# Optimization experiments

Measured on AMD Instinct MI355X. Metric: run time of the kernel, lower is better.

## Reference

```python
import jax, jax.numpy as jnp
import numpy as np

G = 32        # grid points per axis (in_p is a regular [0,1]^3 grid)
M = 8         # half n_modes (n_modes=16 -> keep 8 low + 8 high per dim, 8 in rfft dim)
NL = 4        # fno_n_layers
HID = 64      # fno_hidden_channels
LIFT = 256    # fno_lifting_channels
NOUT = 16384  # number of output query points
RADIUS = 0.033


def setup_inputs() -> dict:
    key = jax.random.key(0)
    ks = jax.random.split(key, 16)
    g = jnp.linspace(0.0, 1.0, G)
    X, Y, Z = jnp.meshgrid(g, g, g, indexing='ij')
    in_p = jnp.stack([X, Y, Z], -1).astype(jnp.float32)            # [G,G,G,3]
    f = jax.random.normal(ks[0], (G, G, G, 3), jnp.float32)        # [G,G,G,3]
    out_p = jax.random.uniform(ks[1], (NOUT, 3), dtype=jnp.float32)

    def lin(k, i, o):
        return jax.random.normal(k, (i, o), jnp.float32) * (float(i) ** -0.5)

    inp = {
        'in_p': in_p, 'out_p': out_p, 'f': f,
        # Lifting MLP: (in_channels+3)=6 -> 256 -> 64
        'lift_w1': lin(ks[2], 6, LIFT), 'lift_b1': jnp.zeros((LIFT,), jnp.float32),
        'lift_w2': lin(ks[3], LIFT, HID), 'lift_b2': jnp.zeros((HID,), jnp.float32),
        # Spectral weights: [layer, corner(4), in, out, M, M, M, (re,im)]
        'spec_w': jax.random.normal(ks[4], (NL, 4, HID, HID, M, M, M, 2), jnp.float32) * 0.02,
        # Linear (soft) skip per layer
        'skip_w': jax.random.normal(ks[5], (NL, HID, HID), jnp.float32) * (float(HID) ** -0.5),
        'skip_b': jnp.zeros((NL, HID), jnp.float32),
        # GNO kernel MLP: 6 -> 512 -> 256 -> 64
        'gno_w1': lin(ks[6], 6, 512), 'gno_b1': jnp.zeros((512,), jnp.float32),
        'gno_w2': lin(ks[7], 512, 256), 'gno_b2': jnp.zeros((256,), jnp.float32),
        'gno_w3': lin(ks[8], 256, HID), 'gno_b3': jnp.zeros((HID,), jnp.float32),
        # Projection: 64 -> 256 -> 1
        'proj_w1': lin(ks[9], HID, 256), 'proj_b1': jnp.zeros((256,), jnp.float32),
        'proj_w2': lin(ks[10], 256, 1), 'proj_b2': jnp.zeros((1,), jnp.float32),
    }
    return inp


def reference(in_p, out_p, f, lift_w1, lift_b1, lift_w2, lift_b2, spec_w,
              skip_w, skip_b, gno_w1, gno_b1, gno_w2, gno_b2, gno_w3, gno_b3,
              proj_w1, proj_b1, proj_w2, proj_b2):
    gelu = lambda x: jax.nn.gelu(x, approximate=False)

    # ---- FNO latent embedding (channels-last) ----
    h = jnp.concatenate([f, in_p], -1)                               # [G,G,G,6]
    h = gelu(h @ lift_w1 + lift_b1) @ lift_w2 + lift_b2              # [G,G,G,HID]

    w = spec_w[..., 0] + 1j * spec_w[..., 1]                         # [NL,4,i,o,M,M,M]
    lo, hi = slice(0, M), slice(-M, None)
    corners = [(lo, lo), (lo, hi), (hi, lo), (hi, hi)]
    sz = slice(0, M)
    for l in range(NL):
        ft = jnp.fft.rfftn(h, axes=(0, 1, 2), norm='forward')        # [G,G,G//2+1,HID]
        out_ft = jnp.zeros_like(ft)
        for c, (sx, sy) in enumerate(corners):
            blk = jnp.einsum('xyzi,ioxyz->xyzo', ft[sx, sy, sz], w[l, c])
            out_ft = out_ft.at[sx, sy, sz].set(blk)
        hs = jnp.fft.irfftn(out_ft, s=(G, G, G), axes=(0, 1, 2), norm='forward')
        h = hs + h @ skip_w[l] + skip_b[l]
        if l < NL - 1:
            h = gelu(h)
    latent = h.reshape(-1, HID)                                      # [G^3, HID]

    # ---- GNO: radius neighbor search on regular grid + gather-MLP-mean ----
    hgrid = 1.0 / (G - 1)
    i0 = jnp.round(out_p * (G - 1)).astype(jnp.int32)                # nearest cell [N,3]
    off = jnp.stack(jnp.meshgrid(*([jnp.arange(-1, 2)] * 3), indexing='ij'), -1).reshape(-1, 3)
    cand = i0[:, None, :] + off[None]                                # [N,27,3]
    inb = jnp.all((cand >= 0) & (cand < G), -1)
    cc = jnp.clip(cand, 0, G - 1)
    flat = (cc[..., 0] * G + cc[..., 1]) * G + cc[..., 2]            # [N,27]
    ycoord = cc.astype(jnp.float32) * hgrid                          # neighbor coords
    d2 = jnp.sum((out_p[:, None, :] - ycoord) ** 2, -1)
    mask = inb & (d2 <= RADIUS * RADIUS)

    # kernel input = cat([y_coords, x_coords]) per edge -> MLP -> k(x,y) [N,27,HID]
    agg = jnp.concatenate([ycoord, jnp.broadcast_to(out_p[:, None, :], ycoord.shape)], -1)
    k = gelu(agg @ gno_w1 + gno_b1)
    k = gelu(k @ gno_w2 + gno_b2)
    k = k @ gno_w3 + gno_b3
    fy = latent[flat]                                                # gather [N,27,HID]
    msk = mask[..., None].astype(k.dtype)
    num = jnp.sum(k * fy * msk, axis=1)
    den = jnp.maximum(jnp.sum(msk, axis=1), 1.0)
    out = num / den                                                  # [N,HID] (mean reduce)

    # ---- Projection ----
    out = gelu(out @ proj_w1 + proj_b1) @ proj_w2 + proj_b2          # [N,1]
    return out
```

## Files before the change

### kernel.cpp

```cpp
#include <hip/hip_runtime.h>
#include <math.h>


#define ECAP 131072

typedef _Float16 f16x8 __attribute__((ext_vector_type(8)));
typedef float f32x4 __attribute__((ext_vector_type(4)));

__device__ __forceinline__ float gelu_f(float x) {
    float t = fabsf(x) * 0.7071067811865475f;
    float k = __builtin_amdgcn_rcpf(1.0f + 0.3275911f * t);
    float e = __expf(-t * t);
    float y = k*(0.254829592f + k*(-0.284496736f + k*(1.421413741f +
              k*(-1.453152027f + k*1.061405429f))));
    float erfv = 1.0f - y * e;
    return 0.5f * x * (1.0f + copysignf(erfv, x));
}

__global__ __launch_bounds__(256) void k_prep(const float* __restrict__ w2,
                                              const float* __restrict__ w3,
                                              const float* __restrict__ w1,
                                              const float* __restrict__ b1,
                                              const float* __restrict__ lw2,
                                              const float* __restrict__ skw,
                                              const float* __restrict__ out_p,
                                              _Float16* __restrict__ w2T,
                                              _Float16* __restrict__ w3T,
                                              _Float16* __restrict__ w1p,
                                              _Float16* __restrict__ l2hi,
                                              _Float16* __restrict__ l2lo,
                                              _Float16* __restrict__ skwH,
                                              _Float16* __restrict__ skwL,
                                              int* __restrict__ counter,
                                              int* __restrict__ baseG,
                                              int* __restrict__ cntG,
                                              int* __restrict__ eFlat,
                                              float* __restrict__ eAgg)
{
    if (blockIdx.x >= 720) {
        int n = (blockIdx.x - 720)*256 + threadIdx.x;
        const float hg = 1.0f/31.0f;
        const float r2 = (float)(0.033*0.033);
        float px = out_p[n*3+0], py = out_p[n*3+1], pz = out_p[n*3+2];
        int ix = (int)rintf(px*31.f), iy = (int)rintf(py*31.f), iz = (int)rintf(pz*31.f);
        unsigned msk = 0; int cnt = 0;
        for (int j = 0; j < 27; ++j) {
            int dx = j/9 - 1, dy = (j/3)%3 - 1, dz = j%3 - 1;
            int cx = ix+dx, cy = iy+dy, cz = iz+dz;
            bool inb = (cx>=0)&&(cx<32)&&(cy>=0)&&(cy<32)&&(cz>=0)&&(cz<32);
            int qx = min(max(cx,0),31), qy = min(max(cy,0),31), qz = min(max(cz,0),31);
            float yx = qx*hg, yy = qy*hg, yz = qz*hg;
            float d2 = (px-yx)*(px-yx) + (py-yy)*(py-yy) + (pz-yz)*(pz-yz);
            if (inb && d2 <= r2) { msk |= 1u<<j; cnt++; }
        }
        int base = atomicAdd(counter, cnt);
        baseG[n] = base; cntG[n] = cnt;
        int k = 0;
        for (int j = 0; j < 27; ++j) if (msk & (1u<<j)) {
            int dx = j/9 - 1, dy = (j/3)%3 - 1, dz = j%3 - 1;
            int cx = ix+dx, cy = iy+dy, cz = iz+dz;
            int e = base + k;
            eFlat[e] = (cx*32 + cy)*32 + cz;
            eAgg[e*6+0] = cx*hg; eAgg[e*6+1] = cy*hg; eAgg[e*6+2] = cz*hg;
            eAgg[e*6+3] = px;    eAgg[e*6+4] = py;    eAgg[e*6+5] = pz;
            ++k;
        }
        return;
    }
    int idx = blockIdx.x*256 + threadIdx.x;
    if (idx < 131072) {
        int k = idx >> 8, n = idx & 255;
        w2T[n*512 + k] = (_Float16)w2[idx];
    } else if (idx < 147456) {
        int j = idx - 131072;
        int k = j >> 6, o = j & 63;
        w3T[o*256 + k] = (_Float16)w3[j];
    } else if (idx < 151552) {
        int j = idx - 147456;
        int k = j >> 3, d = j & 7;
        float v = d < 6 ? w1[d*512 + k] : (d == 6 ? b1[k] : 0.0f);
        w1p[k*8 + d] = (_Float16)v;
    } else if (idx < 167936) {
        int j = idx - 151552;
        int o = j >> 8, k = j & 255;
        float v = lw2[k*64 + o];
        _Float16 hi = (_Float16)v;
        l2hi[j] = hi;
        l2lo[j] = (_Float16)(v - (float)hi);
    } else if (idx < 184320) {
        int j = idx - 167936;
        int l = j >> 12, r = j & 4095;
        int co = r >> 6, ci = r & 63;
        float v = skw[l*4096 + ci*64 + co];
        _Float16 hi = (_Float16)v;
        skwH[j] = hi;
        skwL[j] = (_Float16)(v - (float)hi);
    }
}

__global__ __launch_bounds__(256) void k_lift(
    const float* __restrict__ f, const float* __restrict__ in_p,
    const float* __restrict__ w1, const float* __restrict__ b1,
    const _Float16* __restrict__ l2hi,
    const _Float16* __restrict__ l2lo,
    const float* __restrict__ b2,
    float* __restrict__ h)
{
    __shared__ __align__(16) _Float16 h1hi[64*264];
    __shared__ __align__(16) _Float16 h1lo[64*264];
    __shared__ float w1s[6*256];
    __shared__ float b1s[256];
    float* oT = (float*)h1hi;
    int t = threadIdx.x;
    for (int i = t; i < 1536; i += 256) w1s[i] = w1[i];
    b1s[t] = b1[t];
    int p0 = blockIdx.x * 64;
    int pt = t >> 2, jq = t & 3;
    int p = p0 + pt;
    float x0 = f[p*3+0], x1 = f[p*3+1], x2 = f[p*3+2];
    float x3 = in_p[p*3+0], x4 = in_p[p*3+1], x5 = in_p[p*3+2];
    __syncthreads();
    for (int r = 0; r < 8; ++r) {
        int j0 = jq*64 + r*8;
        f16x8 vh, vl;
        #pragma unroll
        for (int jj = 0; jj < 8; ++jj) {
            int j = j0 + jj;
            float a = b1s[j] + x0*w1s[j] + x1*w1s[256+j] + x2*w1s[512+j]
                    + x3*w1s[768+j] + x4*w1s[1024+j] + x5*w1s[1280+j];
            float g = gelu_f(a);
            _Float16 hi = (_Float16)g;
            vh[jj] = hi;
            vl[jj] = (_Float16)(g - (float)hi);
        }
        *(f16x8*)&h1hi[pt*264 + j0] = vh;
        *(f16x8*)&h1lo[pt*264 + j0] = vl;
    }
    __syncthreads();
    int w = t >> 6, lane = t & 63, l15 = lane & 15, g = lane >> 4;
    f32x4 acc[4];
    #pragma unroll
    for (int nt = 0; nt < 4; ++nt) {
        float bb = b2[nt*16 + l15];
        acc[nt] = (f32x4){bb, bb, bb, bb};
    }
    for (int kk = 0; kk < 8; ++kk) {
        f16x8 ah = *(const f16x8*)&h1hi[(w*16+l15)*264 + kk*32 + g*8];
        f16x8 al = *(const f16x8*)&h1lo[(w*16+l15)*264 + kk*32 + g*8];
        #pragma unroll
        for (int nt = 0; nt < 4; ++nt) {
            f16x8 bh = *(const f16x8*)&l2hi[(nt*16+l15)*256 + kk*32 + g*8];
            f16x8 bl = *(const f16x8*)&l2lo[(nt*16+l15)*256 + kk*32 + g*8];
            acc[nt] = __builtin_amdgcn_mfma_f32_16x16x32_f16(al, bh, acc[nt], 0, 0, 0);
            acc[nt] = __builtin_amdgcn_mfma_f32_16x16x32_f16(ah, bl, acc[nt], 0, 0, 0);
            acc[nt] = __builtin_amdgcn_mfma_f32_16x16x32_f16(ah, bh, acc[nt], 0, 0, 0);
        }
    }
    __syncthreads();
    #pragma unroll
    for (int nt = 0; nt < 4; ++nt)
        #pragma unroll
        for (int r = 0; r < 4; ++r)
            oT[(nt*16 + l15)*68 + w*16 + g*4 + r] = acc[nt][r];
    __syncthreads();
    for (int i = t; i < 4096; i += 256) {
        int c = i >> 6, ptl = i & 63;
        h[(size_t)c*32768 + p0 + ptl] = oT[c*68 + ptl];
    }
}

__global__ __launch_bounds__(256) void k_fwd_zy(const float* __restrict__ h,
                                                float2* __restrict__ F1)
{
    __shared__ float pl[8*1056];
    __shared__ float2 fz[32*73];
    __shared__ float twc[32], tws[32];
    int t = threadIdx.x;
    int x = blockIdx.x >> 3, cg = blockIdx.x & 7;
    for (int i = t; i < 8192; i += 256) {
        int c = i >> 10, yz = i & 1023;
        pl[c*1056 + (yz>>5)*33 + (yz&31)] = h[(cg*8 + c)*32768 + x*1024 + yz];
    }
    if (t < 32) { float th = (float)t*(6.283185307179586f/32.f); twc[t]=cosf(th); tws[t]=sinf(th); }
    __syncthreads();
    {
        int c = t >> 5, y = t & 31;
        float zv[32];
        #pragma unroll
        for (int z = 0; z < 32; ++z) zv[z] = pl[c*1056 + y*33 + z];
        const float inv = 1.0f/32768.0f;
        #pragma unroll
        for (int kz = 0; kz < 8; ++kz) {
            float re = 0.f, im = 0.f;
            #pragma unroll
            for (int z = 0; z < 32; ++z) {
                int ph = (kz*z)&31;
                re += zv[z]*twc[ph];
                im -= zv[z]*tws[ph];
            }
            fz[y*73 + kz*9 + c] = make_float2(re*inv, im*inv);
        }
    }
    __syncthreads();
    #pragma unroll
    for (int ko = 0; ko < 4; ++ko) {
        int idx = ko*256 + t;
        int kyi = idx >> 6, kz = (idx >> 3) & 7, c = idx & 7;
        int ky = kyi < 8 ? kyi : kyi + 16;
        float re = 0.f, im = 0.f;
        for (int y = 0; y < 32; ++y) {
            int ph = (ky*y)&31;
            float cc = twc[ph], ss = tws[ph];
            float2 a = fz[y*73 + kz*9 + c];
            re += a.x*cc + a.y*ss;
            im += a.y*cc - a.x*ss;
        }
        F1[((kyi*8 + kz)*32 + x)*64 + cg*8 + c] = make_float2(re, im);
    }
}

__global__ __launch_bounds__(256) void k_fwd_x(const float2* __restrict__ F1,
                                               float2* __restrict__ Ft)
{
    __shared__ float2 fs[32*65];
    __shared__ float twc[32], tws[32];
    int t = threadIdx.x;
    int kyi = blockIdx.x >> 3, kz = blockIdx.x & 7;
    const float2* src = &F1[(size_t)((kyi*8 + kz)*32)*64];
    for (int i = t; i < 2048; i += 256) fs[(i>>6)*65 + (i&63)] = src[i];
    if (t < 32) { float th = (float)t*(6.283185307179586f/32.f); twc[t]=cosf(th); tws[t]=sinf(th); }
    __syncthreads();
    #pragma unroll
    for (int ko = 0; ko < 4; ++ko) {
        int idx = ko*256 + t;
        int kxi = idx >> 6, ii = idx & 63;
        int kx = kxi < 8 ? kxi : kxi + 16;
        float re = 0.f, im = 0.f;
        for (int xx = 0; xx < 32; ++xx) {
            int ph = (kx*xx)&31;
            float cc = twc[ph], ss = tws[ph];
            float2 a = fs[xx*65 + ii];
            re += a.x*cc + a.y*ss;
            im += a.y*cc - a.x*ss;
        }
        Ft[((kxi*16 + kyi)*8 + kz)*64 + ii] = make_float2(re, im);
    }
}

__global__ __launch_bounds__(256) void k_spec_skip(const float2* __restrict__ Ft,
                                                   const float* __restrict__ spw,
                                                   const float* __restrict__ hold,
                                                   const _Float16* __restrict__ skwH,
                                                   const _Float16* __restrict__ skwL,
                                                   float2* __restrict__ Gt,
                                                   float* __restrict__ hsk,
                                                   int l)
{
    __shared__ float2 ft2[64*65];
    __shared__ __align__(16) _Float16 shi[128*72];
    __shared__ __align__(16) _Float16 slo[128*72];
    int t = threadIdx.x;
    if (blockIdx.x >= 256) {
        int pt0 = (blockIdx.x - 256) * 128;
        for (int i = t; i < 2048; i += 256) {
            int ci = i >> 5, q = i & 31;
            float4 v = *(const float4*)&hold[(size_t)ci*32768 + pt0 + q*4];
            #pragma unroll
            for (int j = 0; j < 4; ++j) {
                float fv = (&v.x)[j];
                _Float16 hi = (_Float16)fv;
                shi[(q*4+j)*72 + ci] = hi;
                slo[(q*4+j)*72 + ci] = (_Float16)(fv - (float)hi);
            }
        }
        __syncthreads();
        int w = t >> 6, lane = t & 63, l15 = lane & 15, g = lane >> 4;
        f32x4 acc[8];
        #pragma unroll
        for (int nt = 0; nt < 8; ++nt) acc[nt] = (f32x4){0.f, 0.f, 0.f, 0.f};
        #pragma unroll
        for (int kk = 0; kk < 2; ++kk) {
            f16x8 ah = *(const f16x8*)&skwH[l*4096 + (w*16+l15)*64 + kk*32 + g*8];
            f16x8 al = *(const f16x8*)&skwL[l*4096 + (w*16+l15)*64 + kk*32 + g*8];
            #pragma unroll
            for (int nt = 0; nt < 8; ++nt) {
                f16x8 bh = *(const f16x8*)&shi[(nt*16+l15)*72 + kk*32 + g*8];
                f16x8 bl = *(const f16x8*)&slo[(nt*16+l15)*72 + kk*32 + g*8];
                acc[nt] = __builtin_amdgcn_mfma_f32_16x16x32_f16(al, bh, acc[nt], 0, 0, 0);
                acc[nt] = __builtin_amdgcn_mfma_f32_16x16x32_f16(ah, bl, acc[nt], 0, 0, 0);
                acc[nt] = __builtin_amdgcn_mfma_f32_16x16x32_f16(ah, bh, acc[nt], 0, 0, 0);
            }
        }
        #pragma unroll
        for (int nt = 0; nt < 8; ++nt)
            #pragma unroll
            for (int r = 0; r < 4; ++r)
                hsk[(size_t)(w*16 + g*4 + r)*32768 + pt0 + nt*16 + l15] = acc[nt][r];
        return;
    }
    int og8 = blockIdx.x >> 5, corner = (blockIdx.x >> 3) & 3, mx = blockIdx.x & 7;
    int kxi = mx + (corner >> 1)*8;
    int kyB = (corner & 1)*8;
    {
        int m = t >> 2, iq = t & 3;
        int my = m >> 3, mz = m & 7;
        int rho = (m >> 1) + ((m & 1) << 5);
        const float2* src = &Ft[(size_t)((kxi*16 + kyB + my)*8 + mz)*64];
        #pragma unroll
        for (int ii = 0; ii < 16; ++ii) {
            int i = iq*16 + ii;
            ft2[rho*65 + i] = src[i];
        }
    }
    __syncthreads();
    int mp = t & 31, oq = t >> 5;
    int o = og8*8 + oq;
    int m0 = 2*mp;
    size_t wbase = (size_t)(l*4 + corner)*4194304 + (size_t)o*1024
                 + (size_t)mx*128 + m0*2;
    float ar0 = 0.f, ai0 = 0.f, ar1 = 0.f, ai1 = 0.f;
    for (int i8 = 0; i8 < 64; i8 += 8) {
        float4 wv[8];
        #pragma unroll
        for (int u = 0; u < 8; ++u)
            wv[u] = *(const float4*)&spw[wbase + (size_t)(i8+u)*65536];
        #pragma unroll
        for (int u = 0; u < 8; ++u) {
            float2 f0 = ft2[mp*65 + i8 + u];
            float2 f1 = ft2[(32 + mp)*65 + i8 + u];
            ar0 += f0.x*wv[u].x - f0.y*wv[u].y;
            ai0 += f0.x*wv[u].y + f0.y*wv[u].x;
            ar1 += f1.x*wv[u].z - f1.y*wv[u].w;
            ai1 += f1.x*wv[u].w + f1.y*wv[u].z;
        }
    }
    size_t gbase = (size_t)(o >> 2)*8192 + (size_t)(corner*8 + mx)*256 + (o & 3);
    Gt[gbase + (size_t)m0*4]       = make_float2(ar0, ai0);
    Gt[gbase + (size_t)(m0+1)*4]   = make_float2(ar1, ai1);
}

__global__ __launch_bounds__(256) void k_inv(const float2* __restrict__ Gt,
                                             const float* __restrict__ hsk,
                                             const float* __restrict__ skb,
                                             float* __restrict__ hnew,
                                             float* __restrict__ latent,
                                             int l)
{
    __shared__ float2 gt[8192];
    __shared__ float2 s1[16*8*4];
    __shared__ float2 s2[32*8*4];
    __shared__ float twc[32], tws[32];
    int t = threadIdx.x;
    int x = blockIdx.x >> 4, og = blockIdx.x & 15;
    const float2* gsrc = &Gt[(size_t)og*8192];
    for (int i = t; i < 8192; i += 256) gt[i] = gsrc[i];
    if (t < 32) { float th = (float)t*(6.283185307179586f/32.f); twc[t]=cosf(th); tws[t]=sinf(th); }
    __syncthreads();
    #pragma unroll
    for (int ko = 0; ko < 2; ++ko) {
        int idx = ko*256 + t;
        int kyi = idx >> 5, kz = (idx >> 2) & 7, o = idx & 3;
        int cy = kyi >> 3, my = kyi & 7;
        float re = 0.f, im = 0.f;
        #pragma unroll
        for (int cxh = 0; cxh < 2; ++cxh) {
            int corner = cxh*2 + cy;
            #pragma unroll
            for (int mxx = 0; mxx < 8; ++mxx) {
                int kxi = cxh*8 + mxx;
                int kx = kxi < 8 ? kxi : kxi + 16;
                int ph = (kx * x) & 31;
                float cc = twc[ph], ss = tws[ph];
                float2 a = gt[((corner*8 + mxx)*64 + my*8 + kz)*4 + o];
                re += a.x*cc - a.y*ss;
                im += a.x*ss + a.y*cc;
            }
        }
        s1[(kyi*8 + kz)*4 + o] = make_float2(re, im);
    }
    __syncthreads();
    #pragma unroll
    for (int ko = 0; ko < 4; ++ko) {
        int idx = ko*256 + t;
        int y = idx >> 5, kz = (idx >> 2) & 7, o = idx & 3;
        float re = 0.f, im = 0.f;
        #pragma unroll
        for (int kyi = 0; kyi < 16; ++kyi) {
            int ky = kyi < 8 ? kyi : kyi + 16;
            int ph = (ky*y) & 31;
            float cc = twc[ph], ss = tws[ph];
            float2 a = s1[(kyi*8 + kz)*4 + o];
            re += a.x*cc - a.y*ss;
            im += a.x*ss + a.y*cc;
        }
        s2[(y*8 + kz)*4 + o] = make_float2(re, im);
    }
    __syncthreads();
    float acc[4][4];
    #pragma unroll
    for (int o = 0; o < 4; ++o) {
        float bb = skb[l*64 + og*4 + o];
        float4 hv = *(const float4*)&hsk[(size_t)(og*4+o)*32768 + x*1024 + t*4];
        acc[0][o] = bb + hv.x; acc[1][o] = bb + hv.y;
        acc[2][o] = bb + hv.z; acc[3][o] = bb + hv.w;
    }
    float outv[4][4];
    #pragma unroll
    for (int pp = 0; pp < 4; ++pp) {
        int pt = t*4 + pp;
        int y = pt >> 5, z = pt & 31;
        #pragma unroll
        for (int o = 0; o < 4; ++o) {
            float s = s2[(y*8)*4 + o].x;
            #pragma unroll
            for (int kz = 1; kz < 8; ++kz) {
                int ph = (kz*z) & 31;
                float2 a = s2[(y*8 + kz)*4 + o];
                s += 2.0f*(a.x*twc[ph] - a.y*tws[ph]);
            }
            float v = s + acc[pp][o];
            outv[pp][o] = (l < 3) ? gelu_f(v) : v;
        }
    }
    if (l < 3) {
        #pragma unroll
        for (int o = 0; o < 4; ++o) {
            float4 w4 = make_float4(outv[0][o], outv[1][o], outv[2][o], outv[3][o]);
            *(float4*)&hnew[(size_t)(og*4 + o)*32768 + x*1024 + t*4] = w4;
        }
    } else {
        #pragma unroll
        for (int pp = 0; pp < 4; ++pp) {
            float4 w4 = make_float4(outv[pp][0], outv[pp][1], outv[pp][2], outv[pp][3]);
            *(float4*)&latent[(size_t)(x*1024 + t*4 + pp)*64 + og*4] = w4;
        }
    }
}

__global__ __launch_bounds__(256, 2) void k_gno_mlp(
    const int* __restrict__ counter,
    const int* __restrict__ eFlat,
    const float* __restrict__ eAgg,
    const _Float16* __restrict__ w1p,
    const _Float16* __restrict__ w2T,
    const float* __restrict__ b2,
    const _Float16* __restrict__ w3T,
    const float* __restrict__ b3,
    const float* __restrict__ latent,
    float* __restrict__ kv)
{
    __shared__ __align__(16) _Float16 h1pool[64*520];
    __shared__ __align__(16) _Float16 w1s[512*8];
    __shared__ float aggs[64][6];
    __shared__ int   flatS[64];
    _Float16* h2h = h1pool;

    int t = threadIdx.x;
    int E = counter[0]; if (E > ECAP) E = ECAP;
    int s = blockIdx.x * 64;
    if (s >= E) return;
    int ne = min(64, E - s);

    for (int i = t; i < 512; i += 256)
        ((int4*)w1s)[i] = ((const int4*)w1p)[i];
    for (int i = t; i < 384; i += 256)
        aggs[i/6][i - (i/6)*6] = (i < ne*6) ? eAgg[(size_t)s*6 + i] : 0.0f;
    if (t < 64) flatS[t] = (t < ne) ? eFlat[s + t] : 0;
    __syncthreads();

    int e = t & 63;
    int w = t >> 6;
    {
        float a0 = aggs[e][0], a1 = aggs[e][1], a2 = aggs[e][2];
        float a3 = aggs[e][3], a4 = aggs[e][4], a5 = aggs[e][5];
        int xk = (e >> 3) & 7;
        #pragma unroll
        for (int ci = 0; ci < 16; ++ci) {
            int c = w*16 + ci;
            f16x8 v;
            #pragma unroll
            for (int jj = 0; jj < 8; ++jj) {
                int k = c*8 + jj;
                f16x8 wv = *(const f16x8*)&w1s[k*8];
                float pre = (float)wv[6]
                    + a0*(float)wv[0] + a1*(float)wv[1] + a2*(float)wv[2]
                    + a3*(float)wv[3] + a4*(float)wv[4] + a5*(float)wv[5];
                v[jj] = (_Float16)gelu_f(pre);
            }
            *(f16x8*)&h1pool[e*520 + ((c ^ xk)*8)] = v;
        }
    }
    __syncthreads();

    int lane = t & 63;
    int l15 = lane & 15, g = lane >> 4;

    f32x4 acc2[4][4];
    #pragma unroll
    for (int nt = 0; nt < 4; ++nt) {
        float bb = b2[w*64 + nt*16 + l15];
        #pragma unroll
        for (int mt = 0; mt < 4; ++mt) acc2[mt][nt] = (f32x4){bb, bb, bb, bb};
    }
    #pragma unroll 4
    for (int kk = 0; kk < 16; ++kk) {
        f16x8 af[4];
        #pragma unroll
        for (int mt = 0; mt < 4; ++mt) {
            int ee = mt*16 + l15;
            af[mt] = *(const f16x8*)&h1pool[ee*520 + (((kk*4 + g) ^ ((ee>>3)&7))*8)];
        }
        #pragma unroll
        for (int nt = 0; nt < 4; ++nt) {
            f16x8 bf = *(const f16x8*)&w2T[(size_t)(w*64 + nt*16 + l15)*512 + kk*32 + g*8];
            #pragma unroll
            for (int mt = 0; mt < 4; ++mt)
                acc2[mt][nt] = __builtin_amdgcn_mfma_f32_16x16x32_f16(af[mt], bf, acc2[mt][nt], 0, 0, 0);
        }
    }
    __syncthreads();
    #pragma unroll
    for (int mt = 0; mt < 4; ++mt)
      #pragma unroll
      for (int nt = 0; nt < 4; ++nt) {
        int n = w*64 + nt*16 + l15;
        #pragma unroll
        for (int r = 0; r < 4; ++r) {
            int m = mt*16 + g*4 + r;
            h2h[m*264 + (((n>>3) ^ (m&7))*8) + (n&7)] = (_Float16)gelu_f(acc2[mt][nt][r]);
        }
      }
    __syncthreads();

    int o = w*16 + l15;
    f32x4 acc3[4];
    { float bb = b3[o];
      #pragma unroll
      for (int mt = 0; mt < 4; ++mt) acc3[mt] = (f32x4){bb, bb, bb, bb}; }
    #pragma unroll 2
    for (int kk2 = 0; kk2 < 8; ++kk2) {
        f16x8 bf = *(const f16x8*)&w3T[(size_t)o*256 + kk2*32 + g*8];
        #pragma unroll
        for (int mt = 0; mt < 4; ++mt) {
            int ee = mt*16 + l15;
            f16x8 af = *(const f16x8*)&h2h[ee*264 + (((kk2*4 + g) ^ (ee&7))*8)];
            acc3[mt] = __builtin_amdgcn_mfma_f32_16x16x32_f16(af, bf, acc3[mt], 0, 0, 0);
        }
    }

    #pragma unroll
    for (int mt = 0; mt < 4; ++mt) {
        #pragma unroll
        for (int r = 0; r < 4; ++r) {
            int ee = mt*16 + g*4 + r;
            if (ee < ne) {
                float fy = latent[(size_t)flatS[ee]*64 + o];
                kv[(size_t)(s + ee)*64 + o] = acc3[mt][r] * fy;
            }
        }
    }
}

__global__ __launch_bounds__(256) void k_project(const int* __restrict__ baseG,
                                                 const int* __restrict__ cntG,
                                                 const float* __restrict__ kv,
                                                 const float* __restrict__ pw1,
                                                 const float* __restrict__ pb1,
                                                 const float* __restrict__ pw2,
                                                 const float* __restrict__ pb2,
                                                 float* __restrict__ outp)
{
    __shared__ float w1s[64*260];
    __shared__ float xT[64*68];
    __shared__ float w2s[256];
    __shared__ float b1s[256];
    __shared__ float red[64*4];
    int t = threadIdx.x;
    int p0 = blockIdx.x * 64;
    for (int i = t; i < 16384; i += 256) {
        int k = i >> 8, o = i & 255;
        w1s[k*260 + o] = pw1[i];
    }
    w2s[t] = pw2[t];
    b1s[t] = pb1[t];
    for (int i = t; i < 4096; i += 256) {
        int ptl = i >> 6, c = i & 63;
        int p = p0 + ptl;
        int base = baseG[p], cnt = cntG[p];
        float acc = 0.f;
        for (int j = 0; j < cnt; ++j) acc += kv[(size_t)(base + j)*64 + c];
        xT[c*68 + ptl] = acc / fmaxf((float)cnt, 1.0f);
    }
    __syncthreads();
    int pr = t & 15, oc0 = t >> 4;
    float psum[4] = {0.f, 0.f, 0.f, 0.f};
    for (int it = 0; it < 4; ++it) {
        int oc = it*16 + oc0;
        float a[4][4];
        #pragma unroll
        for (int pp = 0; pp < 4; ++pp)
            #pragma unroll
            for (int q = 0; q < 4; ++q) a[pp][q] = b1s[oc*4 + q];
        for (int i = 0; i < 64; ++i) {
            float4 xv = *(const float4*)&xT[i*68 + pr*4];
            float4 wv = *(const float4*)&w1s[i*260 + oc*4];
            #pragma unroll
            for (int q = 0; q < 4; ++q) {
                float wq = (&wv.x)[q];
                a[0][q] += xv.x*wq; a[1][q] += xv.y*wq;
                a[2][q] += xv.z*wq; a[3][q] += xv.w*wq;
            }
        }
        #pragma unroll
        for (int pp = 0; pp < 4; ++pp) {
            float s = 0.f;
            #pragma unroll
            for (int q = 0; q < 4; ++q) s += gelu_f(a[pp][q]) * w2s[oc*4 + q];
            psum[pp] += s;
        }
    }
    #pragma unroll
    for (int pp = 0; pp < 4; ++pp) {
        psum[pp] += __shfl_xor(psum[pp], 16, 64);
        psum[pp] += __shfl_xor(psum[pp], 32, 64);
    }
    int lane = t & 63, w = t >> 6;
    if (lane < 16) {
        #pragma unroll
        for (int pp = 0; pp < 4; ++pp) red[(lane*4 + pp)*4 + w] = psum[pp];
    }
    __syncthreads();
    if (t < 64)
        outp[p0 + t] = red[t*4+0] + red[t*4+1] + red[t*4+2] + red[t*4+3] + pb2[0];
}

extern "C" void kernel_launch(void* const* d_in, const int* in_sizes, int n_in,
                              void* d_out, int out_size, void* d_ws, size_t ws_size,
                              hipStream_t stream)
{
    const float* in_p = (const float*)d_in[0];
    const float* outp = (const float*)d_in[1];
    const float* f    = (const float*)d_in[2];
    const float* lw1  = (const float*)d_in[3];
    const float* lb1  = (const float*)d_in[4];
    const float* lw2  = (const float*)d_in[5];
    const float* lb2  = (const float*)d_in[6];
    const float* spw  = (const float*)d_in[7];
    const float* skw  = (const float*)d_in[8];
    const float* skb  = (const float*)d_in[9];
    const float* gw1  = (const float*)d_in[10];
    const float* gb1  = (const float*)d_in[11];
    const float* gw2  = (const float*)d_in[12];
    const float* gb2  = (const float*)d_in[13];
    const float* gw3  = (const float*)d_in[14];
    const float* gb3  = (const float*)d_in[15];
    const float* pw1  = (const float*)d_in[16];
    const float* pb1  = (const float*)d_in[17];
    const float* pw2  = (const float*)d_in[18];
    const float* pb2  = (const float*)d_in[19];

    float* ws   = (float*)d_ws;
    float* buf0 = ws;
    float* buf1 = ws + 2097152;
    float* SC   = ws + 4194304;
    float2* F1 = (float2*)SC;
    float2* Ft = (float2*)(SC + 524288);
    float2* Gt = (float2*)(SC + 786432);
    _Float16* w2T  = (_Float16*)(SC + 1048576);
    _Float16* w3T  = (_Float16*)(SC + 1114112);
    _Float16* w1p  = (_Float16*)(SC + 1122304);
    _Float16* l2hi = (_Float16*)(SC + 1124352);
    _Float16* l2lo = (_Float16*)(SC + 1132544);
    _Float16* skwH = (_Float16*)(SC + 1140736);
    _Float16* skwL = (_Float16*)(SC + 1148928);
    int*   counter = (int*)(SC + 1157120);
    int*   baseG   = (int*)(SC + 1157136);
    int*   cntG    = (int*)(SC + 1173520);
    int*   eFlat   = (int*)(SC + 1189904);
    float* eAgg    = SC + 1320976;
    float* kv      = SC + 2107408;
    float* hsk     = SC + 10496016;

    hipMemsetAsync(counter, 0, sizeof(int), stream);
    k_prep<<<784, 256, 0, stream>>>(gw2, gw3, gw1, gb1, lw2, skw, outp,
                                    w2T, w3T, w1p, l2hi, l2lo, skwH, skwL,
                                    counter, baseG, cntG, eFlat, eAgg);
    k_lift<<<512, 256, 0, stream>>>(f, in_p, lw1, lb1, l2hi, l2lo, lb2, buf0);

    for (int l = 0; l < 4; ++l) {
        const float* hin = (l & 1) ? buf1 : buf0;
        float* hout = (l & 1) ? buf0 : buf1;
        k_fwd_zy<<<256, 256, 0, stream>>>(hin, F1);
        k_fwd_x<<<128, 256, 0, stream>>>(F1, Ft);
        k_spec_skip<<<512, 256, 0, stream>>>(Ft, spw, hin, skwH, skwL, Gt, hsk, l);
        k_inv<<<512, 256, 0, stream>>>(Gt, hsk, skb, hout, buf0, l);
    }

    k_gno_mlp<<<ECAP/64, 256, 0, stream>>>(counter, eFlat, eAgg,
                                           w1p, w2T, gb2, w3T, gb3, buf0, kv);
    k_project<<<256, 256, 0, stream>>>(baseG, cntG, kv, pw1, pb1, pw2, pb2,
                                       (float*)d_out);
}
```

Baseline: 415.7 us.

## Fuse next layer's forward z/y DFT into inverse kernel, split fwd_x blocks

```diff
diff --git a/kernel.cpp b/kernel.cpp
--- a/kernel.cpp
+++ b/kernel.cpp
@@ -222,28 +222,32 @@
 __global__ __launch_bounds__(256) void k_fwd_x(const float2* __restrict__ F1,
                                                float2* __restrict__ Ft)
 {
-    __shared__ float2 fs[32*65];
+    __shared__ float2 fs[32*33];
     __shared__ float twc[32], tws[32];
     int t = threadIdx.x;
-    int kyi = blockIdx.x >> 3, kz = blockIdx.x & 7;
-    const float2* src = &F1[(size_t)((kyi*8 + kz)*32)*64];
-    for (int i = t; i < 2048; i += 256) fs[(i>>6)*65 + (i&63)] = src[i];
+    int b = blockIdx.x;
+    int kyi = b >> 4, kz = (b >> 1) & 7, ih = b & 1;
+    const float2* src = &F1[(size_t)((kyi*8 + kz)*32)*64 + ih*32];
+    for (int i = t; i < 1024; i += 256) {
+        int xx = i >> 5, il = i & 31;
+        fs[xx*33 + il] = src[xx*64 + il];
+    }
     if (t < 32) { float th = (float)t*(6.283185307179586f/32.f); twc[t]=cosf(th); tws[t]=sinf(th); }
     __syncthreads();
     #pragma unroll
-    for (int ko = 0; ko < 4; ++ko) {
+    for (int ko = 0; ko < 2; ++ko) {
         int idx = ko*256 + t;
-        int kxi = idx >> 6, ii = idx & 63;
+        int kxi = idx >> 5, il = idx & 31;
         int kx = kxi < 8 ? kxi : kxi + 16;
         float re = 0.f, im = 0.f;
         for (int xx = 0; xx < 32; ++xx) {
             int ph = (kx*xx)&31;
             float cc = twc[ph], ss = tws[ph];
-            float2 a = fs[xx*65 + ii];
+            float2 a = fs[xx*33 + il];
             re += a.x*cc + a.y*ss;
             im += a.y*cc - a.x*ss;
         }
-        Ft[((kxi*16 + kyi)*8 + kz)*64 + ii] = make_float2(re, im);
+        Ft[((kxi*16 + kyi)*8 + kz)*64 + ih*32 + il] = make_float2(re, im);
     }
 }
 
@@ -256,11 +260,11 @@
                                                    float* __restrict__ hsk,
                                                    int l)
 {
-    __shared__ float2 ft2[64*65];
-    __shared__ __align__(16) _Float16 shi[128*72];
-    __shared__ __align__(16) _Float16 slo[128*72];
+    __shared__ __align__(16) char pool[36864];
     int t = threadIdx.x;
     if (blockIdx.x >= 256) {
+        _Float16* shi = (_Float16*)pool;
+        _Float16* slo = (_Float16*)(pool + 18432);
         int pt0 = (blockIdx.x - 256) * 128;
         for (int i = t; i < 2048; i += 256) {
             int ci = i >> 5, q = i & 31;
@@ -298,6 +302,7 @@
                 hsk[(size_t)(w*16 + g*4 + r)*32768 + pt0 + nt*16 + l15] = acc[nt][r];
         return;
     }
+    float2* ft2 = (float2*)pool;
     int og8 = blockIdx.x >> 5, corner = (blockIdx.x >> 3) & 3, mx = blockIdx.x & 7;
     int kxi = mx + (corner >> 1)*8;
     int kyB = (corner & 1)*8;
@@ -339,28 +344,31 @@
     Gt[gbase + (size_t)(m0+1)*4]   = make_float2(ar1, ai1);
 }
 
-__global__ __launch_bounds__(256) void k_inv(const float2* __restrict__ Gt,
-                                             const float* __restrict__ hsk,
-                                             const float* __restrict__ skb,
-                                             float* __restrict__ hnew,
-                                             float* __restrict__ latent,
-                                             int l)
-{
-    __shared__ float2 gt[8192];
-    __shared__ float2 s1[16*8*4];
-    __shared__ float2 s2[32*8*4];
+__global__ __launch_bounds__(512) void k_inv_zy(const float2* __restrict__ Gt,
+                                                const float* __restrict__ hsk,
+                                                const float* __restrict__ skb,
+                                                float* __restrict__ hnew,
+                                                float* __restrict__ latent,
+                                                float2* __restrict__ F1,
+                                                int l, int do_zy)
+{
+    __shared__ __align__(16) char pool[58368];
     __shared__ float twc[32], tws[32];
+    float2* s1 = (float2*)pool;
+    float2* s2 = (float2*)(pool + 8192);
+    float*  pl = (float*)(pool + 24576);
+    float2* fz = (float2*)pool;
+
     int t = threadIdx.x;
-    int x = blockIdx.x >> 4, og = blockIdx.x & 15;
-    const float2* gsrc = &Gt[(size_t)og*8192];
-    for (int i = t; i < 8192; i += 256) gt[i] = gsrc[i];
+    int x = blockIdx.x >> 3, cg = blockIdx.x & 7;
     if (t < 32) { float th = (float)t*(6.283185307179586f/32.f); twc[t]=cosf(th); tws[t]=sinf(th); }
     __syncthreads();
     #pragma unroll
     for (int ko = 0; ko < 2; ++ko) {
-        int idx = ko*256 + t;
-        int kyi = idx >> 5, kz = (idx >> 2) & 7, o = idx & 3;
+        int idx = ko*512 + t;
+        int kyi = idx >> 6, kz = (idx >> 3) & 7, o = idx & 7;
         int cy = kyi >> 3, my = kyi & 7;
+        const float2* gb = Gt + (size_t)(cg*2 + (o>>2))*8192 + my*32 + kz*4 + (o&3);
         float re = 0.f, im = 0.f;
         #pragma unroll
         for (int cxh = 0; cxh < 2; ++cxh) {
@@ -371,69 +379,114 @@
                 int kx = kxi < 8 ? kxi : kxi + 16;
                 int ph = (kx * x) & 31;
                 float cc = twc[ph], ss = tws[ph];
-                float2 a = gt[((corner*8 + mxx)*64 + my*8 + kz)*4 + o];
+                float2 a = gb[(corner*8 + mxx)*256];
                 re += a.x*cc - a.y*ss;
                 im += a.x*ss + a.y*cc;
             }
         }
-        s1[(kyi*8 + kz)*4 + o] = make_float2(re, im);
+        s1[idx] = make_float2(re, im);
     }
     __syncthreads();
     #pragma unroll
     for (int ko = 0; ko < 4; ++ko) {
-        int idx = ko*256 + t;
-        int y = idx >> 5, kz = (idx >> 2) & 7, o = idx & 3;
+        int idx = ko*512 + t;
+        int y = idx >> 6, kz = (idx >> 3) & 7, o = idx & 7;
         float re = 0.f, im = 0.f;
         #pragma unroll
         for (int kyi = 0; kyi < 16; ++kyi) {
             int ky = kyi < 8 ? kyi : kyi + 16;
             int ph = (ky*y) & 31;
             float cc = twc[ph], ss = tws[ph];
-            float2 a = s1[(kyi*8 + kz)*4 + o];
+            float2 a = s1[kyi*64 + kz*8 + o];
             re += a.x*cc - a.y*ss;
             im += a.x*ss + a.y*cc;
         }
-        s2[(y*8 + kz)*4 + o] = make_float2(re, im);
-    }
-    __syncthreads();
-    float acc[4][4];
-    #pragma unroll
-    for (int o = 0; o < 4; ++o) {
-        float bb = skb[l*64 + og*4 + o];
-        float4 hv = *(const float4*)&hsk[(size_t)(og*4+o)*32768 + x*1024 + t*4];
-        acc[0][o] = bb + hv.x; acc[1][o] = bb + hv.y;
-        acc[2][o] = bb + hv.z; acc[3][o] = bb + hv.w;
-    }
-    float outv[4][4];
-    #pragma unroll
-    for (int pp = 0; pp < 4; ++pp) {
-        int pt = t*4 + pp;
-        int y = pt >> 5, z = pt & 31;
-        #pragma unroll
-        for (int o = 0; o < 4; ++o) {
-            float s = s2[(y*8)*4 + o].x;
-            #pragma unroll
-            for (int kz = 1; kz < 8; ++kz) {
-                int ph = (kz*z) & 31;
-                float2 a = s2[(y*8 + kz)*4 + o];
-                s += 2.0f*(a.x*twc[ph] - a.y*tws[ph]);
-            }
-            float v = s + acc[pp][o];
-            outv[pp][o] = (l < 3) ? gelu_f(v) : v;
-        }
-    }
-    if (l < 3) {
-        #pragma unroll
-        for (int o = 0; o < 4; ++o) {
-            float4 w4 = make_float4(outv[0][o], outv[1][o], outv[2][o], outv[3][o]);
-            *(float4*)&hnew[(size_t)(og*4 + o)*32768 + x*1024 + t*4] = w4;
-        }
-    } else {
-        #pragma unroll
-        for (int pp = 0; pp < 4; ++pp) {
-            float4 w4 = make_float4(outv[pp][0], outv[pp][1], outv[pp][2], outv[pp][3]);
-            *(float4*)&latent[(size_t)(x*1024 + t*4 + pp)*64 + og*4] = w4;
-        }
+        s2[idx] = make_float2(re, im);
+    }
+    __syncthreads();
+    {
+        float outv[2][8];
+        #pragma unroll
+        for (int o = 0; o < 8; ++o) {
+            float bb = skb[l*64 + cg*8 + o];
+            float2 hv = *(const float2*)&hsk[(size_t)(cg*8+o)*32768 + x*1024 + t*2];
+            outv[0][o] = bb + hv.x;
+            outv[1][o] = bb + hv.y;
+        }
+        #pragma unroll
+        for (int pp = 0; pp < 2; ++pp) {
+            int pt = t*2 + pp;
+            int y = pt >> 5, z = pt & 31;
+            #pragma unroll
+            for (int o = 0; o < 8; ++o) {
+                float s = s2[y*64 + o].x;
+                #pragma unroll
+                for (int kz = 1; kz < 8; ++kz) {
+                    int ph = (kz*z) & 31;
+                    float2 a = s2[y*64 + kz*8 + o];
+                    s += 2.0f*(a.x*twc[ph] - a.y*tws[ph]);
+                }
+                float v = s + outv[pp][o];
+                outv[pp][o] = (l < 3) ? gelu_f(v) : v;
+            }
+        }
+        if (l < 3) {
+            #pragma unroll
+            for (int o = 0; o < 8; ++o) {
+                int pt = t*2;
+                int y = pt >> 5, z = pt & 31;
+                pl[o*1056 + y*33 + z]     = outv[0][o];
+                pl[o*1056 + y*33 + z + 1] = outv[1][o];
+                *(float2*)&hnew[(size_t)(cg*8+o)*32768 + x*1024 + pt] =
+                    make_float2(outv[0][o], outv[1][o]);
+            }
+        } else {
+            #pragma unroll
+            for (int pp = 0; pp < 2; ++pp) {
+                int pt = t*2 + pp;
+                float4 w0 = make_float4(outv[pp][0], outv[pp][1], outv[pp][2], outv[pp][3]);
+                float4 w1 = make_float4(outv[pp][4], outv[pp][5], outv[pp][6], outv[pp][7]);
+                *(float4*)&latent[(size_t)(x*1024 + pt)*64 + cg*8]     = w0;
+                *(float4*)&latent[(size_t)(x*1024 + pt)*64 + cg*8 + 4] = w1;
+            }
+        }
+    }
+    if (!do_zy) return;
+    __syncthreads();
+    {
+        int c = t >> 6, y = t & 31, sub = (t >> 5) & 1;
+        float zv[32];
+        #pragma unroll
+        for (int z = 0; z < 32; ++z) zv[z] = pl[c*1056 + y*33 + z];
+        const float inv = 1.0f/32768.0f;
+        #pragma unroll
+        for (int kq = 0; kq < 4; ++kq) {
+            int kz = sub*4 + kq;
+            float re = 0.f, im = 0.f;
+            #pragma unroll
+            for (int z = 0; z < 32; ++z) {
+                int ph = (kz*z)&31;
+                re += zv[z]*twc[ph];
+                im -= zv[z]*tws[ph];
+            }
+            fz[y*73 + kz*9 + c] = make_float2(re*inv, im*inv);
+        }
+    }
+    __syncthreads();
+    #pragma unroll
+    for (int ko = 0; ko < 2; ++ko) {
+        int idx = ko*512 + t;
+        int kyi = idx >> 6, kz = (idx >> 3) & 7, c = idx & 7;
+        int ky = kyi < 8 ? kyi : kyi + 16;
+        float re = 0.f, im = 0.f;
+        for (int y = 0; y < 32; ++y) {
+            int ph = (ky*y)&31;
+            float cc = twc[ph], ss = tws[ph];
+            float2 a = fz[y*73 + kz*9 + c];
+            re += a.x*cc + a.y*ss;
+            im += a.y*cc - a.x*ss;
+        }
+        F1[((kyi*8 + kz)*32 + x)*64 + cg*8 + c] = make_float2(re, im);
     }
 }
 
@@ -687,13 +740,14 @@
                                     counter, baseG, cntG, eFlat, eAgg);
     k_lift<<<512, 256, 0, stream>>>(f, in_p, lw1, lb1, l2hi, l2lo, lb2, buf0);
 
+    k_fwd_zy<<<256, 256, 0, stream>>>(buf0, F1);
     for (int l = 0; l < 4; ++l) {
         const float* hin = (l & 1) ? buf1 : buf0;
         float* hout = (l & 1) ? buf0 : buf1;
-        k_fwd_zy<<<256, 256, 0, stream>>>(hin, F1);
-        k_fwd_x<<<128, 256, 0, stream>>>(F1, Ft);
+        k_fwd_x<<<256, 256, 0, stream>>>(F1, Ft);
         k_spec_skip<<<512, 256, 0, stream>>>(Ft, spw, hin, skwH, skwL, Gt, hsk, l);
-        k_inv<<<512, 256, 0, stream>>>(Gt, hsk, skb, hout, buf0, l);
+        k_inv_zy<<<256, 512, 0, stream>>>(Gt, hsk, skb, hout, buf0, F1,
+                                          l, (l < 3) ? 1 : 0);
     }
 
     k_gno_mlp<<<ECAP/64, 256, 0, stream>>>(counter, eFlat, eAgg,
```

New measurement: 357.7 us. -14.0%, faster.
